# Kernel tuning notes

Hardware: AMD Instinct MI355X
Metric: run time of the kernel (lower is better)

## Reference

```python
import jax, jax.numpy as jnp
import numpy as np

HQ, HKV, D = 16, 2, 128   # num_heads_q, num_heads_kv, head_dim
G = HQ // HKV             # q heads per kv head (repeat_interleave factor)


def setup_inputs() -> dict:
    key = jax.random.key(0)
    ks = jax.random.split(key, 6)
    B, T, C = 2, 2048, 2048
    def w(k, shape):
        return jax.random.normal(k, shape, jnp.float32) * (1.0 / np.sqrt(shape[0]).astype(np.float32))
    x = jax.random.normal(ks[0], (B, T, C), jnp.float32)
    Wq = w(ks[1], (C, HQ * D))
    Wk = w(ks[2], (C, HKV * D))
    Wv = w(ks[3], (C, HKV * D))
    Wo = w(ks[4], (HQ * D, C))
    Wg = w(ks[5], (C, HQ))
    # causal mask: True where attention is disallowed (j > i)
    mask = jnp.triu(jnp.ones((T, T), dtype=bool), k=1)[None, None]  # (1,1,T,T)
    return {"x": x, "mask": mask, "Wq": Wq, "Wk": Wk, "Wv": Wv, "Wo": Wo, "Wg": Wg}


def reference(x, mask, Wq, Wk, Wv, Wo, Wg):
    B, T, C = x.shape
    # repeat_interleave(G, dim=heads) means q head h uses kv head h // G,
    # so group q heads as (HKV, G) instead of materializing repeated K/V.
    q = (x @ Wq).reshape(B, T, HKV, G, D).transpose(0, 2, 3, 1, 4)  # (B,HKV,G,T,D)
    k = (x @ Wk).reshape(B, T, HKV, D).transpose(0, 2, 1, 3)        # (B,HKV,T,D)
    v = (x @ Wv).reshape(B, T, HKV, D).transpose(0, 2, 1, 3)        # (B,HKV,T,D)
    scale = jnp.float32(1.0 / np.sqrt(D))
    scores = jnp.einsum('bkgtd,bksd->bkgts', q, k) * scale          # (B,HKV,G,T,T)
    scores = jnp.where(mask[:, None], jnp.float32(-1e9), scores)    # causal fill
    attn = jax.nn.softmax(scores, axis=-1)
    # post-softmax sigmoid gate, one scalar per (batch, q-head, query token)
    gates = jax.nn.sigmoid(x @ Wg)                                   # (B,T,HQ)
    gates = gates.transpose(0, 2, 1).reshape(B, HKV, G, T)           # (B,HKV,G,T)
    out = jnp.einsum('bkgts,bksd->btkgd', attn * gates[..., None], v)
    out = out.reshape(B, T, HQ * D)
    return out @ Wo
```

## Files before the change

### kernel.cpp

```cpp
#include <hip/hip_runtime.h>
#include <hip/hip_bf16.h>
#include <math.h>

#define HQ 16
#define HKV 2
#define D 128
#define B_SZ 2
#define T_SZ 2048
#define C_SZ 2048
#define QKVN 2688

#define C_Q 0.12753102f
#define C_G 1.44269504f

typedef __attribute__((ext_vector_type(8))) short short8;
typedef __attribute__((ext_vector_type(4))) float floatx4;

static __device__ __forceinline__ float fexp2(float x) {
    return __builtin_amdgcn_exp2f(x);
}

static __device__ __forceinline__ unsigned short f2b(float f) {
    union { float f; unsigned u; } x; x.f = f;
    return (unsigned short)((x.u + 0x7fffu + ((x.u >> 16) & 1u)) >> 16);
}

static __device__ __forceinline__ unsigned int pk2(float a, float b) {
    float2 t; t.x = a; t.y = b;
    __hip_bfloat162 h = __float22bfloat162_rn(t);
    return *(unsigned int*)&h;
}

static __device__ __forceinline__ void load_lds16(const void* g, void* l) {
    __builtin_amdgcn_global_load_lds(
        (const __attribute__((address_space(1))) void*)g,
        (__attribute__((address_space(3))) void*)l,
        16, 0, 0);
}

static __device__ __forceinline__ void tr32(
    const float* __restrict__ in, unsigned short* __restrict__ out,
    int R, int Cc, float premul, int bx, int by, float (*t)[33])
{
    const int bc = bx * 32, br = by * 32;
    const int tid = threadIdx.x;
    const int r = tid >> 3, c4 = (tid & 7) * 4;
    float4 v = *(const float4*)(in + (size_t)(br + r) * Cc + bc + c4);
    t[r][c4 + 0] = v.x; t[r][c4 + 1] = v.y; t[r][c4 + 2] = v.z; t[r][c4 + 3] = v.w;
    __syncthreads();
    ushort4 o;
    o.x = f2b(t[c4 + 0][r] * premul); o.y = f2b(t[c4 + 1][r] * premul);
    o.z = f2b(t[c4 + 2][r] * premul); o.w = f2b(t[c4 + 3][r] * premul);
    *(ushort4*)(out + (size_t)(bc + r) * R + br + c4) = o;
}

__global__ __launch_bounds__(256) void prep_kernel(
    const float* __restrict__ x,  const float* __restrict__ Wq,
    const float* __restrict__ Wk, const float* __restrict__ Wv,
    const float* __restrict__ Wo, const float* __restrict__ Wg,
    unsigned short* __restrict__ xb, unsigned short* __restrict__ Wqkvt,
    unsigned short* __restrict__ Wot)
{
    __shared__ float t[32][33];
    const int bid = blockIdx.x;
    const int tid = threadIdx.x;
    if (bid < 4096) {
        int i = bid * 2048 + tid * 8;
        float4 a = *(const float4*)(x + i);
        float4 b = *(const float4*)(x + i + 4);
        ushort4 o0, o1;
        o0.x = f2b(a.x); o0.y = f2b(a.y); o0.z = f2b(a.z); o0.w = f2b(a.w);
        o1.x = f2b(b.x); o1.y = f2b(b.y); o1.z = f2b(b.z); o1.w = f2b(b.w);
        *(ushort4*)(xb + i) = o0;
        *(ushort4*)(xb + i + 4) = o1;
    } else if (bid < 8192) {
        int n = bid - 4096;
        tr32(Wq, Wqkvt, C_SZ, HQ * D, C_Q, n & 63, n >> 6, t);
    } else if (bid < 8704) {
        int n = bid - 8192;
        tr32(Wk, Wqkvt + (size_t)(HQ * D) * C_SZ, C_SZ, HKV * D, 1.0f, n & 7, n >> 3, t);
    } else if (bid < 9216) {
        int n = bid - 8704;
        tr32(Wv, Wqkvt + (size_t)(HQ * D + HKV * D) * C_SZ, C_SZ, HKV * D, 1.0f, n & 7, n >> 3, t);
    } else if (bid < 13312) {
        int n = bid - 9216;
        tr32(Wo, Wot, HQ * D, C_SZ, 1.0f, n & 63, n >> 6, t);
    } else {
        int k = (bid - 13312) * 256 + tid;
        const float4* wr = (const float4*)(Wg + (size_t)k * 16);
        float4 w0 = wr[0], w1 = wr[1], w2 = wr[2], w3 = wr[3];
        float w[16] = {w0.x, w0.y, w0.z, w0.w, w1.x, w1.y, w1.z, w1.w,
                       w2.x, w2.y, w2.z, w2.w, w3.x, w3.y, w3.z, w3.w};
        unsigned short* out = Wqkvt + (size_t)(HQ * D + 2 * HKV * D) * C_SZ;
        #pragma unroll
        for (int h = 0; h < 16; ++h)
            out[(size_t)h * C_SZ + k] = f2b(w[h] * C_G);
    }
}

template<int BM>
__global__ __launch_bounds__(512, 2) void gemm8p(
    const unsigned short* __restrict__ A, const unsigned short* __restrict__ Bt,
    float* __restrict__ Cf, unsigned short* __restrict__ Cb,
    unsigned short* __restrict__ Vt, int Nreal, int K, int out_bf16)
{
    constexpr int MT = BM / 32;
    constexpr int MH = MT / 2;
    constexpr int LA = BM / 128;
    constexpr int AUNIT = (BM / 2) * 64;
    constexpr int BUNIT = 8192;
    constexpr int BUF = 2 * AUNIT + 2 * BUNIT;
    constexpr int VM = LA + 4;
    __shared__ __align__(16) unsigned short SM[2][BUF];

    const int tid = threadIdx.x;
    const int lane = tid & 63, wave = tid >> 6;
    const int l15 = lane & 15, quad = lane >> 4;
    const int wm = wave >> 2, wn = wave & 3;
    const int NT = K >> 6;

    const int nwg = (int)(gridDim.x * gridDim.y);
    int flat = (int)(blockIdx.y * gridDim.x + blockIdx.x);
    const int cpx = nwg >> 3;
    flat = (flat & 7) * cpx + (flat >> 3);
    const int bm0 = (flat / (int)gridDim.x) * BM;
    const int bn0 = (flat % (int)gridDim.x) * 256;

    const int rr = tid >> 3;
    const int cb8 = ((tid & 7) ^ (rr & 7)) << 3;
    unsigned aoff[2][LA], boff[2][2];
    #pragma unroll
    for (int mh = 0; mh < 2; ++mh)
        #pragma unroll
        for (int j = 0; j < LA; ++j) {
            int row_l = j * 64 + rr;
            int grow;
            if (BM == 256) grow = bm0 + (row_l >> 6) * 128 + mh * 64 + (row_l & 63);
            else           grow = bm0 + (row_l >> 5) * 64  + mh * 32 + (row_l & 31);
            aoff[mh][j] = (unsigned)((grow * K + cb8) * 2);
        }
    #pragma unroll
    for (int nh = 0; nh < 2; ++nh)
        #pragma unroll
        for (int j = 0; j < 2; ++j) {
            int row_l = j * 64 + rr;
            int gnr = bn0 + (row_l >> 5) * 64 + nh * 32 + (row_l & 31);
            boff[nh][j] = (unsigned)((gnr * K + cb8) * 2);
        }

    floatx4 zero = {0.f, 0.f, 0.f, 0.f};
    floatx4 acc[MT][4];
    #pragma unroll
    for (int i = 0; i < MT; ++i)
        #pragma unroll
        for (int j = 0; j < 4; ++j) acc[i][j] = zero;

    auto STAGE_A = [&](int b, int mh, int t) {
        #pragma unroll
        for (int j = 0; j < LA; ++j)
            load_lds16((const char*)A + aoff[mh][j] + (size_t)t * 128,
                       &SM[b][mh * AUNIT + (j * 512 + wave * 64) * 8]);
    };
    auto STAGE_B = [&](int b, int nh, int t) {
        #pragma unroll
        for (int j = 0; j < 2; ++j)
            load_lds16((const char*)Bt + boff[nh][j] + (size_t)t * 128,
                       &SM[b][2 * AUNIT + nh * BUNIT + (j * 512 + wave * 64) * 8]);
    };

    short8 fa[MH][2], fb[4][2];
    auto RD_A = [&](int b, int mh) {
        const unsigned short* Sa = &SM[b][mh * AUNIT];
        #pragma unroll
        for (int i = 0; i < MH; ++i) {
            const int row_l = wm * (BM / 4) + i * 16 + l15;
            #pragma unroll
            for (int kk = 0; kk < 2; ++kk)
                fa[i][kk] = *(const short8*)&Sa[row_l * 64 +
                    ((((kk << 2) + quad) ^ (l15 & 7)) << 3)];
        }
    };
    auto RD_Bh = [&](int b, int nh) {
        const unsigned short* Sb = &SM[b][2 * AUNIT + nh * BUNIT];
        #pragma unroll
        for (int s = 0; s < 2; ++s) {
            const int row_l = wn * 32 + s * 16 + l15;
            #pragma unroll
            for (int kk = 0; kk < 2; ++kk)
                fb[nh * 2 + s][kk] = *(const short8*)&Sb[row_l * 64 +
                    ((((kk << 2) + quad) ^ (l15 & 7)) << 3)];
        }
    };
    auto MMQ = [&](int mh, int nh) {
        __builtin_amdgcn_s_setprio(1);
        #pragma unroll
        for (int i = 0; i < MH; ++i)
            #pragma unroll
            for (int s = 0; s < 2; ++s)
                #pragma unroll
                for (int kk = 0; kk < 2; ++kk)
                    acc[mh * MH + i][nh * 2 + s] = __builtin_amdgcn_mfma_f32_16x16x32_bf16(
                        fa[i][kk], fb[nh * 2 + s][kk], acc[mh * MH + i][nh * 2 + s], 0, 0, 0);
        __builtin_amdgcn_s_setprio(0);
    };

    STAGE_A(0, 0, 0); STAGE_B(0, 0, 0); STAGE_B(0, 1, 0); STAGE_A(0, 1, 0);
    if (NT > 1) { STAGE_A(1, 0, 1); STAGE_B(1, 0, 1); STAGE_B(1, 1, 1); }
    asm volatile("s_waitcnt vmcnt(%0)" :: "n"(VM));
    __builtin_amdgcn_s_barrier();

    #pragma unroll 2
    for (int t = 0; t < NT; ++t) {
        const int b = t & 1;
        RD_A(b, 0); RD_Bh(b, 0);
        if (t + 1 < NT) STAGE_A(b ^ 1, 1, t + 1);
        asm volatile("s_waitcnt lgkmcnt(8)");
        __builtin_amdgcn_s_barrier();
        asm volatile("s_waitcnt lgkmcnt(0)");
        MMQ(0, 0);
        __builtin_amdgcn_s_barrier();
        RD_Bh(b, 1);
        if (t + 2 < NT) STAGE_A(b, 0, t + 2);
        __builtin_amdgcn_s_barrier();
        asm volatile("s_waitcnt lgkmcnt(0)");
        MMQ(0, 1);
        __builtin_amdgcn_s_barrier();
        RD_A(b, 1);
        if (t + 2 < NT) STAGE_B(b, 0, t + 2);
        __builtin_amdgcn_s_barrier();
        asm volatile("s_waitcnt lgkmcnt(0)");
        MMQ(1, 1);
        __builtin_amdgcn_s_barrier();
        if (t + 2 < NT) {
            STAGE_B(b, 1, t + 2);
            asm volatile("s_waitcnt vmcnt(%0)" :: "n"(VM));
        } else {
            asm volatile("s_waitcnt vmcnt(0)");
        }
        __builtin_amdgcn_s_barrier();
        MMQ(1, 0);
        __builtin_amdgcn_s_barrier();
    }

    if (BM == 256 && Vt != nullptr && bn0 == 2304) {
        unsigned short (*Ct)[264] = (unsigned short(*)[264])SM;
        const int bb = bm0 >> 11;
        const int tl = bm0 & 2047;
        #pragma unroll
        for (int v = 0; v < 4; ++v) {
            __syncthreads();
            if (wn == v) {
                #pragma unroll
                for (int mt = 0; mt < MT; ++mt)
                    #pragma unroll
                    for (int nt = 0; nt < 4; ++nt)
                        #pragma unroll
                        for (int r = 0; r < 4; ++r)
                            Ct[nt * 16 + l15][wm * (BM / 2) + mt * 16 + quad * 4 + r] =
                                f2b(acc[mt][nt][r]);
            }
            __syncthreads();
            int row = tid >> 3, c0 = (tid & 7) * 32;
            unsigned short* dst = Vt + ((size_t)bb * (HKV * D) + v * 64 + row) * T_SZ
                                     + tl + c0;
            const unsigned short* src = &Ct[row][c0];
            short8 s0 = *(const short8*)(src + 0);
            short8 s1 = *(const short8*)(src + 8);
            short8 s2 = *(const short8*)(src + 16);
            short8 s3 = *(const short8*)(src + 24);
            *(short8*)(dst + 0)  = s0; *(short8*)(dst + 8)  = s1;
            *(short8*)(dst + 16) = s2; *(short8*)(dst + 24) = s3;
        }
        return;
    }

    #pragma unroll
    for (int mt = 0; mt < MT; ++mt)
        #pragma unroll
        for (int nt = 0; nt < 4; ++nt) {
            const int n = bn0 + wn * 64 + nt * 16 + l15;
            if (n < Nreal) {
                #pragma unroll
                for (int r = 0; r < 4; ++r) {
                    const int m = bm0 + wm * (BM / 2) + mt * 16 + quad * 4 + r;
                    if (out_bf16) Cb[(size_t)m * Nreal + n] = f2b(acc[mt][nt][r]);
                    else          Cf[(size_t)m * Nreal + n] = acc[mt][nt][r];
                }
            }
        }
}

__global__ __launch_bounds__(512) void attn_mfma(
    const unsigned short* __restrict__ QKV, const unsigned short* __restrict__ Vt,
    unsigned short* __restrict__ Ob)
{
    __shared__ __align__(16) unsigned short SMEM[2 * 8192 + 2 * 8192 + 128 * 72];
    unsigned short* Ks = SMEM;
    unsigned short* Vs = SMEM + 16384;
    unsigned short* Ps = SMEM + 32768;
    unsigned short* Lo = SMEM;

    const int bh = blockIdx.x;
    const int j = (int)gridDim.y - 1 - (int)blockIdx.y;
    const int b = bh >> 4, h = bh & 15, kvh = h >> 3;
    const int tid = threadIdx.x;
    const int lane = tid & 63, w = tid >> 6;
    const int l15 = lane & 15, quad = lane >> 4;
    const int q_local = w * 16 + l15;
    const int qw  = j * 2 + (q_local >> 6);
    const int qhi = j * 2 + 1;
    const float BIAS = 32.0f;

    short8 aq[4];
    {
        const unsigned short* qp = QKV + (size_t)(b * T_SZ + j * 128 + q_local) * QKVN
                                       + h * D + quad * 8;
        #pragma unroll
        for (int kd = 0; kd < 4; ++kd) aq[kd] = *(const short8*)(qp + kd * 32);
    }

    const unsigned short* kg[2];
    const unsigned short* vg[2];
    #pragma unroll
    for (int it = 0; it < 2; ++it) {
        int Bi = it * 512 + tid;
        int kr = Bi >> 4, kc = ((Bi & 15) ^ (kr & 15)) * 8;
        kg[it] = QKV + (size_t)(b * T_SZ + kr) * QKVN + HQ * D + kvh * D + kc;
        int vr = Bi >> 3, vc = ((Bi & 7) ^ (vr & 7)) * 8;
        vg[it] = Vt + (size_t)((b * HKV + kvh) * D + vr) * T_SZ + vc;
    }

    floatx4 zero = {0.f, 0.f, 0.f, 0.f};
    floatx4 oacc[8];
    #pragma unroll
    for (int dt = 0; dt < 8; ++dt) oacc[dt] = zero;
    float l_part = 0.f;

    auto STAGE = [&](int kt, int buf) {
        #pragma unroll
        for (int it = 0; it < 2; ++it) {
            load_lds16(kg[it] + (size_t)kt * 64 * QKVN,
                       &Ks[buf * 8192 + (it * 512 + w * 64) * 8]);
            load_lds16(vg[it] + kt * 64,
                       &Vs[buf * 8192 + (it * 512 + w * 64) * 8]);
        }
    };

    STAGE(0, 0);
    for (int kt = 0; kt <= qhi; ++kt) {
        const int cur = kt & 1;
        __syncthreads();
        if (kt < qhi) STAGE(kt + 1, cur ^ 1);
        if (kt > qw) continue;

        const unsigned short* Kc = Ks + cur * 8192;
        const unsigned short* Vc = Vs + cur * 8192;

        floatx4 sacc[4];
        #pragma unroll
        for (int nt = 0; nt < 4; ++nt) sacc[nt] = zero;
        #pragma unroll
        for (int kd = 0; kd < 4; ++kd)
            #pragma unroll
            for (int nt = 0; nt < 4; ++nt) {
                short8 ak = *(const short8*)&Kc[((nt * 16 + l15) * 16 + ((kd * 4 + quad) ^ l15)) * 8];
                sacc[nt] = __builtin_amdgcn_mfma_f32_16x16x32_bf16(ak, aq[kd], sacc[nt], 0, 0, 0);
            }

        float p[4][4];
        if (kt == qw) {
            const int qm = q_local & 63;
            #pragma unroll
            for (int nt = 0; nt < 4; ++nt)
                #pragma unroll
                for (int r = 0; r < 4; ++r) {
                    float e = fexp2(sacc[nt][r] - BIAS);
                    p[nt][r] = (nt * 16 + quad * 4 + r > qm) ? 0.f : e;
                }
        } else {
            #pragma unroll
            for (int nt = 0; nt < 4; ++nt)
                #pragma unroll
                for (int r = 0; r < 4; ++r)
                    p[nt][r] = fexp2(sacc[nt][r] - BIAS);
        }
        #pragma unroll
        for (int nt = 0; nt < 4; ++nt) {
            l_part += (p[nt][0] + p[nt][1]) + (p[nt][2] + p[nt][3]);
            uint2 pw;
            pw.x = pk2(p[nt][0], p[nt][1]);
            pw.y = pk2(p[nt][2], p[nt][3]);
            *(uint2*)&Ps[(w * 16 + l15) * 72 + nt * 16 + quad * 4] = pw;
        }

        #pragma unroll
        for (int kk = 0; kk < 2; ++kk) {
            short8 bp = *(const short8*)&Ps[(w * 16 + l15) * 72 + kk * 32 + quad * 8];
            #pragma unroll
            for (int dt = 0; dt < 8; ++dt) {
                short8 av = *(const short8*)&Vc[((dt * 16 + l15) * 8 + ((kk * 4 + quad) ^ (l15 & 7))) * 8];
                oacc[dt] = __builtin_amdgcn_mfma_f32_16x16x32_bf16(av, bp, oacc[dt], 0, 0, 0);
            }
        }
    }

    float l = l_part;
    l += __shfl_xor(l, 16);
    l += __shfl_xor(l, 32);

    __syncthreads();
    {
        int token = b * T_SZ + j * 128 + q_local;
        unsigned short gl = QKV[(size_t)token * QKVN + HQ * D + HKV * D * 2 + h];
        union { unsigned u; float f; } gx; gx.u = ((unsigned)gl) << 16;
        float g = 1.0f / (1.0f + fexp2(-gx.f));
        float f = g / l;
        #pragma unroll
        for (int dt = 0; dt < 8; ++dt) {
            uint2 ov;
            ov.x = pk2(oacc[dt][0] * f, oacc[dt][1] * f);
            ov.y = pk2(oacc[dt][2] * f, oacc[dt][3] * f);
            *(uint2*)&Lo[(size_t)q_local * 136 + dt * 16 + quad * 4] = ov;
        }
    }
    __syncthreads();
    {
        int row = tid >> 2, c0 = (tid & 3) * 32;
        size_t tok = (size_t)(b * T_SZ + j * 128 + row);
        unsigned short* op = Ob + tok * (HQ * D) + h * D + c0;
        const unsigned short* lp = &Lo[(size_t)row * 136 + c0];
        short8 v0 = *(const short8*)(lp + 0);
        short8 v1 = *(const short8*)(lp + 8);
        short8 v2 = *(const short8*)(lp + 16);
        short8 v3 = *(const short8*)(lp + 24);
        *(short8*)(op + 0)  = v0; *(short8*)(op + 8)  = v1;
        *(short8*)(op + 16) = v2; *(short8*)(op + 24) = v3;
    }
}

extern "C" void kernel_launch(void* const* d_in, const int* in_sizes, int n_in,
                              void* d_out, int out_size, void* d_ws, size_t ws_size,
                              hipStream_t stream) {
    const float* x  = (const float*)d_in[0];
    const float* Wq = (const float*)d_in[2];
    const float* Wk = (const float*)d_in[3];
    const float* Wv = (const float*)d_in[4];
    const float* Wo = (const float*)d_in[5];
    const float* Wg = (const float*)d_in[6];
    float* out = (float*)d_out;

    const size_t KB = 1ull << 10;
    char* p = (char*)d_ws;
    unsigned short* xb    = (unsigned short*)(p);
    unsigned short* Ob    = xb;
    unsigned short* Wqkvt = (unsigned short*)(p + 16384 * KB);
    unsigned short* Wot   = (unsigned short*)(p + 27136 * KB);
    unsigned short* QKV   = (unsigned short*)(p + 35328 * KB);
    unsigned short* Vt    = (unsigned short*)(p + 56832 * KB);
    const int BT = B_SZ * T_SZ;

    prep_kernel<<<dim3(13320), 256, 0, stream>>>(x, Wq, Wk, Wv, Wo, Wg, xb, Wqkvt, Wot);

    gemm8p<256><<<dim3(11, BT / 256), 512, 0, stream>>>(
        xb, Wqkvt, nullptr, QKV, Vt, QKVN, C_SZ, 1);

    attn_mfma<<<dim3(B_SZ * HQ, T_SZ / 128), 512, 0, stream>>>(QKV, Vt, Ob);

    gemm8p<128><<<dim3(8, BT / 128), 512, 0, stream>>>(
        Ob, Wot, out, nullptr, nullptr, C_SZ, HQ * D, 0);
}
```

Measured before the change: 278.7 us.

## Pair short and long causal query tiles per attention block for load balance

After: 296.9 us. +6.5%, slower.

```diff
diff --git a/kernel.cpp b/kernel.cpp
--- a/kernel.cpp
+++ b/kernel.cpp
@@ -294,29 +294,36 @@
     const unsigned short* __restrict__ QKV, const unsigned short* __restrict__ Vt,
     unsigned short* __restrict__ Ob)
 {
-    __shared__ __align__(16) unsigned short SMEM[2 * 8192 + 2 * 8192 + 128 * 72];
+    __shared__ __align__(16) unsigned short SMEM[2 * 8192 + 2 * 8192 + 2 * 128 * 72];
     unsigned short* Ks = SMEM;
     unsigned short* Vs = SMEM + 16384;
     unsigned short* Ps = SMEM + 32768;
     unsigned short* Lo = SMEM;
 
     const int bh = blockIdx.x;
-    const int j = (int)gridDim.y - 1 - (int)blockIdx.y;
+    const int jA = (int)blockIdx.y;
+    const int jB = 15 - jA;
     const int b = bh >> 4, h = bh & 15, kvh = h >> 3;
     const int tid = threadIdx.x;
     const int lane = tid & 63, w = tid >> 6;
     const int l15 = lane & 15, quad = lane >> 4;
     const int q_local = w * 16 + l15;
-    const int qw  = j * 2 + (q_local >> 6);
-    const int qhi = j * 2 + 1;
+    const int qwA  = jA * 2 + (q_local >> 6);
+    const int qwB  = jB * 2 + (q_local >> 6);
+    const int qhiB = jB * 2 + 1;
     const float BIAS = 32.0f;
 
-    short8 aq[4];
+    short8 aqA[4], aqB[4];
     {
-        const unsigned short* qp = QKV + (size_t)(b * T_SZ + j * 128 + q_local) * QKVN
+        const unsigned short* qa = QKV + (size_t)(b * T_SZ + jA * 128 + q_local) * QKVN
                                        + h * D + quad * 8;
-        #pragma unroll
-        for (int kd = 0; kd < 4; ++kd) aq[kd] = *(const short8*)(qp + kd * 32);
+        const unsigned short* qb = QKV + (size_t)(b * T_SZ + jB * 128 + q_local) * QKVN
+                                       + h * D + quad * 8;
+        #pragma unroll
+        for (int kd = 0; kd < 4; ++kd) {
+            aqA[kd] = *(const short8*)(qa + kd * 32);
+            aqB[kd] = *(const short8*)(qb + kd * 32);
+        }
     }
 
     const unsigned short* kg[2];
@@ -331,10 +338,10 @@
     }
 
     floatx4 zero = {0.f, 0.f, 0.f, 0.f};
-    floatx4 oacc[8];
-    #pragma unroll
-    for (int dt = 0; dt < 8; ++dt) oacc[dt] = zero;
-    float l_part = 0.f;
+    floatx4 oA[8], oB[8];
+    #pragma unroll
+    for (int dt = 0; dt < 8; ++dt) { oA[dt] = zero; oB[dt] = zero; }
+    float lA = 0.f, lB = 0.f;
 
     auto STAGE = [&](int kt, int buf) {
         #pragma unroll
@@ -347,94 +354,132 @@
     };
 
     STAGE(0, 0);
-    for (int kt = 0; kt <= qhi; ++kt) {
+    for (int kt = 0; kt <= qhiB; ++kt) {
         const int cur = kt & 1;
         __syncthreads();
-        if (kt < qhi) STAGE(kt + 1, cur ^ 1);
-        if (kt > qw) continue;
+        if (kt < qhiB) STAGE(kt + 1, cur ^ 1);
+        if (kt > qwB) continue;
+        const bool actA = (kt <= qwA);
 
         const unsigned short* Kc = Ks + cur * 8192;
         const unsigned short* Vc = Vs + cur * 8192;
 
-        floatx4 sacc[4];
-        #pragma unroll
-        for (int nt = 0; nt < 4; ++nt) sacc[nt] = zero;
+        floatx4 sA[4], sB[4];
+        #pragma unroll
+        for (int nt = 0; nt < 4; ++nt) { sA[nt] = zero; sB[nt] = zero; }
         #pragma unroll
         for (int kd = 0; kd < 4; ++kd)
             #pragma unroll
             for (int nt = 0; nt < 4; ++nt) {
                 short8 ak = *(const short8*)&Kc[((nt * 16 + l15) * 16 + ((kd * 4 + quad) ^ l15)) * 8];
-                sacc[nt] = __builtin_amdgcn_mfma_f32_16x16x32_bf16(ak, aq[kd], sacc[nt], 0, 0, 0);
-            }
-
-        float p[4][4];
-        if (kt == qw) {
-            const int qm = q_local & 63;
-            #pragma unroll
-            for (int nt = 0; nt < 4; ++nt)
-                #pragma unroll
-                for (int r = 0; r < 4; ++r) {
-                    float e = fexp2(sacc[nt][r] - BIAS);
-                    p[nt][r] = (nt * 16 + quad * 4 + r > qm) ? 0.f : e;
-                }
-        } else {
-            #pragma unroll
-            for (int nt = 0; nt < 4; ++nt)
-                #pragma unroll
-                for (int r = 0; r < 4; ++r)
-                    p[nt][r] = fexp2(sacc[nt][r] - BIAS);
-        }
-        #pragma unroll
-        for (int nt = 0; nt < 4; ++nt) {
-            l_part += (p[nt][0] + p[nt][1]) + (p[nt][2] + p[nt][3]);
-            uint2 pw;
-            pw.x = pk2(p[nt][0], p[nt][1]);
-            pw.y = pk2(p[nt][2], p[nt][3]);
-            *(uint2*)&Ps[(w * 16 + l15) * 72 + nt * 16 + quad * 4] = pw;
+                if (actA) sA[nt] = __builtin_amdgcn_mfma_f32_16x16x32_bf16(ak, aqA[kd], sA[nt], 0, 0, 0);
+                sB[nt] = __builtin_amdgcn_mfma_f32_16x16x32_bf16(ak, aqB[kd], sB[nt], 0, 0, 0);
+            }
+
+        const int qm = q_local & 63;
+        if (actA) {
+            float p[4][4];
+            if (kt == qwA) {
+                #pragma unroll
+                for (int nt = 0; nt < 4; ++nt)
+                    #pragma unroll
+                    for (int r = 0; r < 4; ++r) {
+                        float e = fexp2(sA[nt][r] - BIAS);
+                        p[nt][r] = (nt * 16 + quad * 4 + r > qm) ? 0.f : e;
+                    }
+            } else {
+                #pragma unroll
+                for (int nt = 0; nt < 4; ++nt)
+                    #pragma unroll
+                    for (int r = 0; r < 4; ++r)
+                        p[nt][r] = fexp2(sA[nt][r] - BIAS);
+            }
+            #pragma unroll
+            for (int nt = 0; nt < 4; ++nt) {
+                lA += (p[nt][0] + p[nt][1]) + (p[nt][2] + p[nt][3]);
+                uint2 pw;
+                pw.x = pk2(p[nt][0], p[nt][1]);
+                pw.y = pk2(p[nt][2], p[nt][3]);
+                *(uint2*)&Ps[(w * 16 + l15) * 72 + nt * 16 + quad * 4] = pw;
+            }
+        }
+        {
+            float p[4][4];
+            if (kt == qwB) {
+                #pragma unroll
+                for (int nt = 0; nt < 4; ++nt)
+                    #pragma unroll
+                    for (int r = 0; r < 4; ++r) {
+                        float e = fexp2(sB[nt][r] - BIAS);
+                        p[nt][r] = (nt * 16 + quad * 4 + r > qm) ? 0.f : e;
+                    }
+            } else {
+                #pragma unroll
+                for (int nt = 0; nt < 4; ++nt)
+                    #pragma unroll
+                    for (int r = 0; r < 4; ++r)
+                        p[nt][r] = fexp2(sB[nt][r] - BIAS);
+            }
+            #pragma unroll
+            for (int nt = 0; nt < 4; ++nt) {
+                lB += (p[nt][0] + p[nt][1]) + (p[nt][2] + p[nt][3]);
+                uint2 pw;
+                pw.x = pk2(p[nt][0], p[nt][1]);
+                pw.y = pk2(p[nt][2], p[nt][3]);
+                *(uint2*)&Ps[128 * 72 + (w * 16 + l15) * 72 + nt * 16 + quad * 4] = pw;
+            }
         }
 
         #pragma unroll
         for (int kk = 0; kk < 2; ++kk) {
-            short8 bp = *(const short8*)&Ps[(w * 16 + l15) * 72 + kk * 32 + quad * 8];
+            short8 bpA, bpB;
+            if (actA) bpA = *(const short8*)&Ps[(w * 16 + l15) * 72 + kk * 32 + quad * 8];
+            bpB = *(const short8*)&Ps[128 * 72 + (w * 16 + l15) * 72 + kk * 32 + quad * 8];
             #pragma unroll
             for (int dt = 0; dt < 8; ++dt) {
                 short8 av = *(const short8*)&Vc[((dt * 16 + l15) * 8 + ((kk * 4 + quad) ^ (l15 & 7))) * 8];
-                oacc[dt] = __builtin_amdgcn_mfma_f32_16x16x32_bf16(av, bp, oacc[dt], 0, 0, 0);
-            }
-        }
-    }
-
-    float l = l_part;
-    l += __shfl_xor(l, 16);
-    l += __shfl_xor(l, 32);
-
-    __syncthreads();
-    {
-        int token = b * T_SZ + j * 128 + q_local;
-        unsigned short gl = QKV[(size_t)token * QKVN + HQ * D + HKV * D * 2 + h];
-        union { unsigned u; float f; } gx; gx.u = ((unsigned)gl) << 16;
-        float g = 1.0f / (1.0f + fexp2(-gx.f));
-        float f = g / l;
-        #pragma unroll
-        for (int dt = 0; dt < 8; ++dt) {
-            uint2 ov;
-            ov.x = pk2(oacc[dt][0] * f, oacc[dt][1] * f);
-            ov.y = pk2(oacc[dt][2] * f, oacc[dt][3] * f);
-            *(uint2*)&Lo[(size_t)q_local * 136 + dt * 16 + quad * 4] = ov;
-        }
-    }
-    __syncthreads();
-    {
-        int row = tid >> 2, c0 = (tid & 3) * 32;
-        size_t tok = (size_t)(b * T_SZ + j * 128 + row);
-        unsigned short* op = Ob + tok * (HQ * D) + h * D + c0;
-        const unsigned short* lp = &Lo[(size_t)row * 136 + c0];
-        short8 v0 = *(const short8*)(lp + 0);
-        short8 v1 = *(const short8*)(lp + 8);
-        short8 v2 = *(const short8*)(lp + 16);
-        short8 v3 = *(const short8*)(lp + 24);
-        *(short8*)(op + 0)  = v0; *(short8*)(op + 8)  = v1;
-        *(short8*)(op + 16) = v2; *(short8*)(op + 24) = v3;
+                if (actA) oA[dt] = __builtin_amdgcn_mfma_f32_16x16x32_bf16(av, bpA, oA[dt], 0, 0, 0);
+                oB[dt] = __builtin_amdgcn_mfma_f32_16x16x32_bf16(av, bpB, oB[dt], 0, 0, 0);
+            }
+        }
+    }
+
+    lA += __shfl_xor(lA, 16); lA += __shfl_xor(lA, 32);
+    lB += __shfl_xor(lB, 16); lB += __shfl_xor(lB, 32);
+
+    #pragma unroll
+    for (int s = 0; s < 2; ++s) {
+        const int js = s ? jB : jA;
+        const floatx4* oo = s ? oB : oA;
+        const float ls = s ? lB : lA;
+        __syncthreads();
+        {
+            int token = b * T_SZ + js * 128 + q_local;
+            unsigned short gl = QKV[(size_t)token * QKVN + HQ * D + HKV * D * 2 + h];
+            union { unsigned u; float f; } gx; gx.u = ((unsigned)gl) << 16;
+            float g = 1.0f / (1.0f + fexp2(-gx.f));
+            float f = g / ls;
+            #pragma unroll
+            for (int dt = 0; dt < 8; ++dt) {
+                uint2 ov;
+                ov.x = pk2(oo[dt][0] * f, oo[dt][1] * f);
+                ov.y = pk2(oo[dt][2] * f, oo[dt][3] * f);
+                *(uint2*)&Lo[(size_t)q_local * 136 + dt * 16 + quad * 4] = ov;
+            }
+        }
+        __syncthreads();
+        {
+            int row = tid >> 2, c0 = (tid & 3) * 32;
+            size_t tok = (size_t)(b * T_SZ + js * 128 + row);
+            unsigned short* op = Ob + tok * (HQ * D) + h * D + c0;
+            const unsigned short* lp = &Lo[(size_t)row * 136 + c0];
+            short8 v0 = *(const short8*)(lp + 0);
+            short8 v1 = *(const short8*)(lp + 8);
+            short8 v2 = *(const short8*)(lp + 16);
+            short8 v3 = *(const short8*)(lp + 24);
+            *(short8*)(op + 0)  = v0; *(short8*)(op + 8)  = v1;
+            *(short8*)(op + 16) = v2; *(short8*)(op + 24) = v3;
+        }
     }
 }
 
@@ -464,7 +509,7 @@
     gemm8p<256><<<dim3(11, BT / 256), 512, 0, stream>>>(
         xb, Wqkvt, nullptr, QKV, Vt, QKVN, C_SZ, 1);
 
-    attn_mfma<<<dim3(B_SZ * HQ, T_SZ / 128), 512, 0, stream>>>(QKV, Vt, Ob);
+    attn_mfma<<<dim3(B_SZ * HQ, 8), 512, 0, stream>>>(QKV, Vt, Ob);
 
     gemm8p<128><<<dim3(8, BT / 128), 512, 0, stream>>>(
         Ob, Wot, out, nullptr, nullptr, C_SZ, HQ * D, 0);
```
